# Performance work log

Measured on AMD Instinct MI355X. Metric: run time of the kernel, lower is better.

The kernel has to match this reference:

```python
import jax, jax.numpy as jnp
import numpy as np

N = 100000   # nodes
E = 600000   # edges
D = 128      # input = hidden = output dim
L = 3        # GNN layers
C = 40       # num_classes
EPS = 1e-5   # BatchNorm eps


def setup_inputs() -> dict:
    key = jax.random.key(0)
    ks = jax.random.split(key, 8)
    x = jax.random.normal(ks[0], (N, D), jnp.float32)
    edge_index = jax.random.randint(ks[1], (2, E), 0, N, jnp.int32)
    # GCNConv weights per layer (Glorot-ish scale), bias zeros
    Ws = jax.random.normal(ks[2], (L, D, D), jnp.float32) / np.sqrt(D)
    bs = jnp.zeros((L, D), jnp.float32)
    # BatchNorm affine params
    gammas = jnp.ones((L, D), jnp.float32)
    betas = jnp.zeros((L, D), jnp.float32)
    # PReLU single slope per layer (torch default init 0.25)
    prelu_a = jnp.full((L,), 0.25, jnp.float32)
    # classification head: Linear(D,D) -> ReLU -> Linear(D,C)
    Wh1 = jax.random.normal(ks[3], (D, D), jnp.float32) / np.sqrt(D)
    bh1 = jnp.zeros((D,), jnp.float32)
    Wh2 = jax.random.normal(ks[4], (D, C), jnp.float32) / np.sqrt(D)
    bh2 = jnp.zeros((C,), jnp.float32)
    return dict(x=x, edge_index=edge_index, Ws=Ws, bs=bs, gammas=gammas,
                betas=betas, prelu_a=prelu_a, Wh1=Wh1, bh1=bh1, Wh2=Wh2, bh2=bh2)


def _gcn_conv(h, src, dst, norm, W, b):
    # PyG GCNConv: out_i = sum_{j->i} norm_ij * (x_j W) + b  (self-loops already in src/dst)
    m = (h @ W)[src] * norm[:, None]          # [E+N, D_out]
    return jax.ops.segment_sum(m, dst, num_segments=N) + b


def reference(x, edge_index, Ws, bs, gammas, betas, prelu_a, Wh1, bh1, Wh2, bh2):
    # add self-loops + symmetric normalization (computed once; same graph each layer)
    loops = jnp.arange(N, dtype=edge_index.dtype)
    src = jnp.concatenate([edge_index[0], loops])
    dst = jnp.concatenate([edge_index[1], loops])
    deg = jax.ops.segment_sum(jnp.ones_like(dst, jnp.float32), dst, num_segments=N)
    dinv = jax.lax.rsqrt(jnp.maximum(deg, 1.0))  # deg >= 1 thanks to self-loops
    norm = dinv[src] * dinv[dst]                 # [E+N]

    h = x
    for l in range(L):
        h = _gcn_conv(h, src, dst, norm, Ws[l], bs[l])
        # BatchNorm in training mode: batch statistics over nodes
        mu = h.mean(axis=0)
        var = h.var(axis=0)
        h = (h - mu) * jax.lax.rsqrt(var + EPS) * gammas[l] + betas[l]
        # PReLU
        h = jnp.where(h > 0, h, prelu_a[l] * h)

    embeddings = h
    logits = jax.nn.relu(embeddings @ Wh1 + bh1) @ Wh2 + bh2
    out = jnp.argmax(logits, axis=1)
    return embeddings, logits, out
```

## Files before the change

### kernel.cpp

```cpp
#include <hip/hip_runtime.h>
#include <hip/hip_bf16.h>
#include <cstddef>

#define N_NODES 100000
#define N_EDGES 600000
#define DD 128
#define LL 3
#define CC 40
#define BN_EPS 1e-5f

typedef __attribute__((ext_vector_type(8))) short bfrag;
typedef __attribute__((ext_vector_type(4))) float f32x4;

__device__ __forceinline__ float ldf(const void* p, long i, int f32) {
    return f32 ? ((const float*)p)[i] : __bfloat162float(((const __hip_bfloat16*)p)[i]);
}
__device__ __forceinline__ void stf(void* p, long i, float v, int f32) {
    if (f32) ((float*)p)[i] = v;
    else     ((__hip_bfloat16*)p)[i] = __float2bfloat16(v);
}

__device__ __forceinline__ unsigned short f2bf(float f) {
    unsigned u = __float_as_uint(f);
    unsigned r = (u + 0x7fffu + ((u >> 16) & 1u)) >> 16;
    return (unsigned short)r;
}
__device__ __forceinline__ float bf2f(unsigned short h) {
    return __uint_as_float(((unsigned)h) << 16);
}

__device__ __forceinline__ void gload_lds16(const unsigned short* g, unsigned short* l) {
    __builtin_amdgcn_global_load_lds((const __attribute__((address_space(1))) unsigned int*)g,
                                     (__attribute__((address_space(3))) unsigned int*)l, 16, 0, 0);
}

__global__ __launch_bounds__(256) void k_detect(const void* __restrict__ x, int* __restrict__ dflag) {
    __shared__ int s[256];
    int t = threadIdx.x;
    const __hip_bfloat16* xb = (const __hip_bfloat16*)x;
    int bad = 0;
    for (int i = t; i < 4096; i += 256) {
        float v = __bfloat162float(xb[i]);
        float a = fabsf(v);
        if (!(a < 1e6f)) bad++;
        else if (v != 0.f && a < 1e-30f) bad++;
    }
    s[t] = bad; __syncthreads();
    for (int off = 128; off > 0; off >>= 1) {
        if (t < off) s[t] += s[t + off];
        __syncthreads();
    }
    if (t == 0) *dflag = (s[0] > 64) ? 1 : 0;
}

__global__ __launch_bounds__(256) void k_packw(const void* __restrict__ Ws, const void* __restrict__ Wh1,
                                               unsigned short* __restrict__ Wp,
                                               const int* __restrict__ dflag) {
    int f = *dflag;
    int u = blockIdx.x * 256 + threadIdx.x;
    int mat = u >> 14;
    int r = u & 16383;
    int k = r >> 7, c = r & 127;
    float wv = (mat < 3) ? ldf(Ws, (long)mat * 16384 + r, f) : ldf(Wh1, r, f);
    unsigned short hi = f2bf(wv);
    float r1 = wv - bf2f(hi);
    unsigned short mid = f2bf(r1);
    float r2 = r1 - bf2f(mid);
    unsigned short lo = f2bf(r2);
    int n = c >> 4, ks = k >> 5, j = k & 7;
    int lanep = (c & 15) | (((k >> 3) & 3) << 4);
    long base = (long)mat * 49152 + (long)((n * 4 + ks) * 3) * 512 + lanep * 8 + j;
    Wp[base] = hi;
    Wp[base + 512] = mid;
    Wp[base + 1024] = lo;
}


__global__ __launch_bounds__(256) void k_init(int* cnt, int* fpos, int* rowptr, float* stats) {
    int i = blockIdx.x * 256 + threadIdx.x;
    if (i < N_NODES) { cnt[i] = 0; fpos[i] = 0; }
    if (i < 6 * DD) stats[i] = 0.f;
    if (i == 0) rowptr[N_NODES] = N_EDGES;
}

__global__ __launch_bounds__(256) void k_count(const int* __restrict__ ei, int* __restrict__ cnt) {
    int e = blockIdx.x * 256 + threadIdx.x;
    if (e < N_EDGES) atomicAdd(&cnt[ei[N_EDGES + e]], 1);
}

__global__ __launch_bounds__(256) void k_scan1(const int* __restrict__ cnt, int* __restrict__ rowptr,
                                               int* __restrict__ bsum, float* __restrict__ dinv) {
    __shared__ int s[256];
    int t = threadIdx.x;
    int i = blockIdx.x * 256 + t;
    int v = (i < N_NODES) ? cnt[i] : 0;
    if (i < N_NODES) dinv[i] = 1.f / sqrtf((float)(1 + v));
    s[t] = v; __syncthreads();
    for (int off = 1; off < 256; off <<= 1) {
        int x = (t >= off) ? s[t - off] : 0;
        __syncthreads();
        s[t] += x; __syncthreads();
    }
    if (i < N_NODES) rowptr[i] = s[t] - v;
    if (t == 255) bsum[blockIdx.x] = s[255];
}

__global__ __launch_bounds__(512) void k_scan2(int* bsum, int nb) {
    __shared__ int s[512];
    int t = threadIdx.x;
    int v = (t < nb) ? bsum[t] : 0;
    s[t] = v; __syncthreads();
    for (int off = 1; off < 512; off <<= 1) {
        int x = (t >= off) ? s[t - off] : 0;
        __syncthreads();
        s[t] += x; __syncthreads();
    }
    if (t < nb) bsum[t] = s[t] - v;
}

__global__ __launch_bounds__(256) void k_scan3(int* rowptr, const int* __restrict__ bsum) {
    int i = blockIdx.x * 256 + threadIdx.x;
    if (i < N_NODES) rowptr[i] += bsum[blockIdx.x];
}

__global__ __launch_bounds__(256) void k_fill(const int* __restrict__ ei, int* __restrict__ fpos,
                                              const int* __restrict__ rowptr, int2* __restrict__ adjw,
                                              const float* __restrict__ dinv) {
    int e = blockIdx.x * 256 + threadIdx.x;
    if (e < N_EDGES) {
        int s = ei[e];
        int d = ei[N_EDGES + e];
        int p = atomicAdd(&fpos[d], 1);
        adjw[rowptr[d] + p] = make_int2(s, __float_as_int(dinv[s]));
    }
}

__device__ __forceinline__ float4 load_row4(const void* __restrict__ src, long row, int q, int f) {
    if (f) {
        return ((const float4*)src)[row * 32 + q];
    } else {
        uint2 u = ((const uint2*)src)[row * 32 + q];
        float4 v;
        v.x = __uint_as_float(u.x << 16);
        v.y = __uint_as_float(u.x & 0xffff0000u);
        v.z = __uint_as_float(u.y << 16);
        v.w = __uint_as_float(u.y & 0xffff0000u);
        return v;
    }
}

__device__ __forceinline__ float4 bn4(float4 v, float4 sc, float4 sh, float al) {
    float y;
    y = fmaf(v.x, sc.x, sh.x); v.x = (y > 0.f) ? y : al * y;
    y = fmaf(v.y, sc.y, sh.y); v.y = (y > 0.f) ? y : al * y;
    y = fmaf(v.z, sc.z, sh.z); v.z = (y > 0.f) ? y : al * y;
    y = fmaf(v.w, sc.w, sh.w); v.w = (y > 0.f) ? y : al * y;
    return v;
}


__global__ __launch_bounds__(256) void k_agg(const void* __restrict__ src,
                                             const int* __restrict__ rowptr,
                                             const int2* __restrict__ adjw,
                                             const float* __restrict__ dinv,
                                             const float* __restrict__ stats,
                                             const void* __restrict__ gam,
                                             const void* __restrict__ bet,
                                             const void* __restrict__ pa,
                                             int bnl,
                                             float* __restrict__ outp,
                                             const int* __restrict__ dflag) {
    __shared__ float s_bn[260];
    int f = *dflag;
    int tid = threadIdx.x;
    bool useBN = (stats != nullptr);
    if (useBN) {
        if (tid < 128) {
            const float invn = 1.f / (float)N_NODES;
            float mean = stats[tid] * invn;
            float varv = stats[128 + tid] * invn - mean * mean;
            float s = ldf(gam, (long)bnl * DD + tid, f) / sqrtf(varv + BN_EPS);
            s_bn[tid] = s;
            s_bn[128 + tid] = ldf(bet, (long)bnl * DD + tid, f) - mean * s;
        }
        if (tid == 0) s_bn[256] = ldf(pa, bnl, f);
        __syncthreads();
    }

    int lane = tid & 63;
    int h = lane >> 5;
    int q = lane & 31;
    int i = blockIdx.x * 4 + (tid >> 6);
    if (i >= N_NODES) return;

    float4 sc = make_float4(1.f, 1.f, 1.f, 1.f);
    float4 sh = make_float4(0.f, 0.f, 0.f, 0.f);
    float al = 0.f;
    if (useBN) {
        sc = ((const float4*)s_bn)[q];
        sh = ((const float4*)(s_bn + 128))[q];
        al = s_bn[256];
    }

    float di = dinv[i];
    int e0 = rowptr[i], e1 = rowptr[i + 1];

    float a0 = 0.f, a1 = 0.f, a2 = 0.f, a3 = 0.f;
    if (h == 0) {
        float4 v = load_row4(src, i, q, f);
        if (useBN) v = bn4(v, sc, sh, al);
        a0 = di * v.x; a1 = di * v.y; a2 = di * v.z; a3 = di * v.w;
    }

    for (int base = e0; base < e1; base += 64) {
        int m = e1 - base; if (m > 64) m = 64;
        int2 aw = (lane < m) ? adjw[base + lane] : make_int2(0, 0);
        int ajl = aw.x;
        float wl = __int_as_float(aw.y);
        for (int t = 0; t < m; t += 4) {
            int s0 = t + h;     if (s0 > 63) s0 = 63;
            int s1 = t + 2 + h; if (s1 > 63) s1 = 63;
            int j0 = __shfl(ajl, s0), j1 = __shfl(ajl, s1);
            float w0 = __shfl(wl, s0), w1 = __shfl(wl, s1);
            float4 v0 = load_row4(src, j0, q, f);
            float4 v1 = load_row4(src, j1, q, f);
            if (useBN) {
                v0 = bn4(v0, sc, sh, al);
                v1 = bn4(v1, sc, sh, al);
            }
            a0 += w0 * v0.x + w1 * v1.x;
            a1 += w0 * v0.y + w1 * v1.y;
            a2 += w0 * v0.z + w1 * v1.z;
            a3 += w0 * v0.w + w1 * v1.w;
        }
    }

    a0 += __shfl_xor(a0, 32);
    a1 += __shfl_xor(a1, 32);
    a2 += __shfl_xor(a2, 32);
    a3 += __shfl_xor(a3, 32);

    if (h == 0) {
        float4 r = make_float4(di * a0, di * a1, di * a2, di * a3);
        ((float4*)outp)[(size_t)i * 32 + q] = r;
    }
}


__global__ __launch_bounds__(256, 3) void k_gemm2(const float* __restrict__ A,
                                                  const unsigned short* __restrict__ Wp,
                                                  const void* __restrict__ bias, long boff,
                                                  const float* __restrict__ statsA,
                                                  const void* __restrict__ gam,
                                                  const void* __restrict__ bet,
                                                  const void* __restrict__ pa, int bnl,
                                                  float* __restrict__ stats,
                                                  float* __restrict__ Cout,
                                                  void* __restrict__ embp, int relu,
                                                  const int* __restrict__ dflag) {
    __shared__ unsigned short Wl[24576];
    __shared__ float red[1024];
    int f = *dflag;
    int tid = threadIdx.x;
    int lane = tid & 63;
    int w = tid >> 6;
    int lr = lane & 15;
    int lg = lane >> 4;
    int rowbase = blockIdx.x * 64 + w * 16;
    int arow = rowbase + lr;
    bool rowok = arow < N_NODES;

    #pragma unroll
    for (int u = 0; u < 12; ++u) {
        int chunk = w * 12 + u;
        gload_lds16(Wp + chunk * 512 + lane * 8, &Wl[chunk * 512]);
    }

    float bcol[8];
    #pragma unroll
    for (int n = 0; n < 8; ++n)
        bcol[n] = bias ? ldf(bias, boff + n * 16 + lr, f) : 0.f;

    float alA = statsA ? ldf(pa, bnl, f) : 0.f;
    const float invn = 1.f / (float)N_NODES;

    bfrag ah[4], am[4], alo[4];
    const float4* A4 = (const float4*)A;
    #pragma unroll
    for (int ks = 0; ks < 4; ++ks) {
        int k0 = ks * 32 + lg * 8;
        float xv[8];
        if (rowok) {
            long bi = (long)arow * 32 + (k0 >> 2);
            float4 x0 = A4[bi], x1 = A4[bi + 1];
            xv[0] = x0.x; xv[1] = x0.y; xv[2] = x0.z; xv[3] = x0.w;
            xv[4] = x1.x; xv[5] = x1.y; xv[6] = x1.z; xv[7] = x1.w;
        } else {
            #pragma unroll
            for (int e = 0; e < 8; ++e) xv[e] = 0.f;
        }
        if (statsA) {
            #pragma unroll
            for (int e = 0; e < 8; ++e) {
                int c = k0 + e;
                float mean = statsA[c] * invn;
                float varv = statsA[128 + c] * invn - mean * mean;
                float s = ldf(gam, (long)bnl * DD + c, f) / sqrtf(varv + BN_EPS);
                float y = fmaf(xv[e], s, ldf(bet, (long)bnl * DD + c, f) - mean * s);
                xv[e] = (y > 0.f) ? y : alA * y;
            }
        }
        bfrag hfr, mfr, lfr;
        #pragma unroll
        for (int e = 0; e < 8; ++e) {
            unsigned short hb2 = f2bf(xv[e]);
            float r1 = xv[e] - bf2f(hb2);
            unsigned short mb2 = f2bf(r1);
            float r2 = r1 - bf2f(mb2);
            hfr[e] = (short)hb2;
            mfr[e] = (short)mb2;
            lfr[e] = (short)f2bf(r2);
        }
        ah[ks] = hfr; am[ks] = mfr; alo[ks] = lfr;
        if (embp && rowok) {
            if (f) {
                ((float4*)embp)[(long)arow * 32 + (k0 >> 2)]     = make_float4(xv[0], xv[1], xv[2], xv[3]);
                ((float4*)embp)[(long)arow * 32 + (k0 >> 2) + 1] = make_float4(xv[4], xv[5], xv[6], xv[7]);
            } else {
                uint4 pk;
                pk.x = (unsigned)(unsigned short)hfr[0] | ((unsigned)(unsigned short)hfr[1] << 16);
                pk.y = (unsigned)(unsigned short)hfr[2] | ((unsigned)(unsigned short)hfr[3] << 16);
                pk.z = (unsigned)(unsigned short)hfr[4] | ((unsigned)(unsigned short)hfr[5] << 16);
                pk.w = (unsigned)(unsigned short)hfr[6] | ((unsigned)(unsigned short)hfr[7] << 16);
                ((uint4*)embp)[(long)arow * 16 + (k0 >> 3)] = pk;
            }
        }
    }

    #pragma unroll
    for (int h = 0; h < 2; ++h) {
        if (h) {
            __syncthreads();
            #pragma unroll
            for (int u = 0; u < 12; ++u) {
                int chunk = w * 12 + u;
                gload_lds16(Wp + 24576 + chunk * 512 + lane * 8, &Wl[chunk * 512]);
            }
        }
        __syncthreads();

        #pragma unroll
        for (int nn = 0; nn < 4; ++nn) {
            int n = h * 4 + nn;
            f32x4 accn = (f32x4){0.f, 0.f, 0.f, 0.f};
            #pragma unroll
            for (int ks = 0; ks < 4; ++ks) {
                int base = ((nn * 4 + ks) * 3) * 512 + lane * 8;
                bfrag bh = *(const bfrag*)&Wl[base];
                bfrag bm = *(const bfrag*)&Wl[base + 512];
                bfrag bl = *(const bfrag*)&Wl[base + 1024];
                accn = __builtin_amdgcn_mfma_f32_16x16x32_bf16(ah[ks],  bh, accn, 0, 0, 0);
                accn = __builtin_amdgcn_mfma_f32_16x16x32_bf16(am[ks],  bh, accn, 0, 0, 0);
                accn = __builtin_amdgcn_mfma_f32_16x16x32_bf16(ah[ks],  bm, accn, 0, 0, 0);
                accn = __builtin_amdgcn_mfma_f32_16x16x32_bf16(am[ks],  bm, accn, 0, 0, 0);
                accn = __builtin_amdgcn_mfma_f32_16x16x32_bf16(alo[ks], bh, accn, 0, 0, 0);
                accn = __builtin_amdgcn_mfma_f32_16x16x32_bf16(ah[ks],  bl, accn, 0, 0, 0);
            }
            float ls = 0.f, lq = 0.f;
            int colb = n * 16 + lr;
            #pragma unroll
            for (int reg = 0; reg < 4; ++reg) {
                int r2 = rowbase + lg * 4 + reg;
                if (r2 < N_NODES) {
                    float o = accn[reg] + bcol[n];
                    if (relu) o = fmaxf(o, 0.f);
                    Cout[(long)r2 * 128 + colb] = o;
                    ls += o;
                    lq += o * o;
                }
            }
            if (stats) {
                ls += __shfl_xor(ls, 16); ls += __shfl_xor(ls, 32);
                lq += __shfl_xor(lq, 16); lq += __shfl_xor(lq, 32);
                if (lane < 16) {
                    red[w * 256 + n * 16 + lane] = ls;
                    red[w * 256 + 128 + n * 16 + lane] = lq;
                }
            }
        }
    }

    if (stats) {
        __syncthreads();
        float t = red[tid] + red[256 + tid] + red[512 + tid] + red[768 + tid];
        atomicAdd(&stats[tid], t);
    }
}


__global__ __launch_bounds__(256) void k_head(const float* __restrict__ Hd, const void* __restrict__ W2,
                                              const void* __restrict__ b2,
                                              void* __restrict__ out_base,
                                              const int* __restrict__ dflag) {
    __shared__ float Wl[128][40];
    __shared__ float bl[40];
    __shared__ float rv[32][8];
    __shared__ int ri[32][8];
    int f = *dflag;
    int tid = threadIdx.x;
    for (int u = tid; u < 128 * 40; u += 256) Wl[u / 40][u % 40] = ldf(W2, u, f);
    if (tid < 40) bl[tid] = ldf(b2, tid, f);
    __syncthreads();
    int rl = tid >> 3, g = tid & 7;
    long r = (long)blockIdx.x * 32 + rl;
    float acc[5];
    #pragma unroll
    for (int j = 0; j < 5; ++j) acc[j] = bl[g * 5 + j];
    for (int k = 0; k < 128; ++k) {
        float h = Hd[r * 128 + k];
        #pragma unroll
        for (int j = 0; j < 5; ++j) acc[j] += h * Wl[k][g * 5 + j];
    }
    float best = acc[0]; int bi = 0;
    #pragma unroll
    for (int j = 1; j < 5; ++j)
        if (acc[j] > best) { best = acc[j]; bi = j; }
    const long LOG_OFF = (long)N_NODES * DD;
    const long ARG_OFF = (long)N_NODES * (DD + CC);
    #pragma unroll
    for (int j = 0; j < 5; ++j) stf(out_base, LOG_OFF + r * 40 + g * 5 + j, acc[j], f);
    rv[rl][g] = best; ri[rl][g] = g * 5 + bi;
    __syncthreads();
    if (tid < 32) {
        long row = (long)blockIdx.x * 32 + tid;
        float bb = rv[tid][0]; int bbi = ri[tid][0];
        #pragma unroll
        for (int g2 = 1; g2 < 8; ++g2)
            if (rv[tid][g2] > bb) { bb = rv[tid][g2]; bbi = ri[tid][g2]; }
        stf(out_base, ARG_OFF + row, (float)bbi, f);
    }
}


extern "C" void kernel_launch(void* const* d_in, const int* in_sizes, int n_in,
                              void* d_out, int out_size, void* d_ws, size_t ws_size,
                              hipStream_t stream) {
    const void* x   = d_in[0];
    const int* ei   = (const int*)d_in[1];
    const void* Ws  = d_in[2];
    const void* bs  = d_in[3];
    const void* gam = d_in[4];
    const void* bet = d_in[5];
    const void* pa  = d_in[6];
    const void* Wh1 = d_in[7];
    const void* bh1 = d_in[8];
    const void* Wh2 = d_in[9];
    const void* bh2 = d_in[10];

    char* w = (char*)d_ws;
    int* cnt     = (int*)w;    w += sizeof(int) * N_NODES;
    int* fpos    = (int*)w;    w += sizeof(int) * N_NODES;
    int* rowptr  = (int*)w;    w += sizeof(int) * (N_NODES + 4);
    int2* adjw   = (int2*)w;   w += sizeof(int2) * N_EDGES;
    int* bsum    = (int*)w;    w += sizeof(int) * 512;
    int* dflag   = (int*)w;    w += sizeof(int) * 4;
    float* dinv  = (float*)w;  w += sizeof(float) * N_NODES;
    float* stats = (float*)w;  w += sizeof(float) * (6 * DD);
    unsigned short* Wp = (unsigned short*)w; w += sizeof(unsigned short) * 4 * 49152;
    float* bufA  = (float*)w;  w += sizeof(float) * (size_t)N_NODES * DD;
    float* bufB  = (float*)w;  w += sizeof(float) * (size_t)N_NODES * DD;

    const int scanBlocks = (N_NODES + 255) / 256;
    const int edgeBlocks = (N_EDGES + 255) / 256;
    const int gemmBlocks = (N_NODES + 63) / 64;
    const int aggBlocks  = (N_NODES + 3) / 4;

    k_detect<<<1, 256, 0, stream>>>(x, dflag);
    k_packw<<<256, 256, 0, stream>>>(Ws, Wh1, Wp, dflag);
    k_init<<<scanBlocks, 256, 0, stream>>>(cnt, fpos, rowptr, stats);
    k_count<<<edgeBlocks, 256, 0, stream>>>(ei, cnt);
    k_scan1<<<scanBlocks, 256, 0, stream>>>(cnt, rowptr, bsum, dinv);
    k_scan2<<<1, 512, 0, stream>>>(bsum, scanBlocks);
    k_scan3<<<scanBlocks, 256, 0, stream>>>(rowptr, bsum);
    k_fill<<<edgeBlocks, 256, 0, stream>>>(ei, fpos, rowptr, adjw, dinv);

    for (int l = 0; l < LL; ++l) {
        const void* src = (l == 0) ? x : (const void*)bufB;
        const float* st = (l == 0) ? nullptr : (stats + (l - 1) * 256);
        k_agg<<<aggBlocks, 256, 0, stream>>>(src, rowptr, adjw, dinv, st, gam, bet, pa,
                                             l - 1, bufA, dflag);
        k_gemm2<<<gemmBlocks, 256, 0, stream>>>(bufA, Wp + (size_t)l * 49152, bs, (long)l * DD,
                                                nullptr, gam, bet, pa, 0,
                                                stats + l * 256, bufB, nullptr, 0, dflag);
    }

    k_gemm2<<<gemmBlocks, 256, 0, stream>>>(bufB, Wp + (size_t)3 * 49152, bh1, 0,
                                            stats + 2 * 256, gam, bet, pa, 2,
                                            nullptr, bufA, d_out, 1, dflag);
    k_head<<<(N_NODES / 32), 256, 0, stream>>>(bufA, Wh2, bh2, d_out, dflag);
}
```

Measured before the change: 672.0 us.

## Move bf16x3 split into aggregation producer and add separate BN split kernel

The aggregation kernel now writes its output already split into three bf16 planes (hi/mid/lo) instead of fp32, so the GEMM loads ready MFMA fragments directly and skips the per-row conversion. The final BN+PReLU and the embedding write move out of the head GEMM into a new elementwise k_split kernel. The GEMM also uses two accumulators to break MFMA dependency chains, and keeps per-column stats in registers, reusing the weight LDS for the reduction. In exchange it adds one kernel launch, and the intermediate buffer grows from 4 to 6 bytes per element.

```diff
diff --git a/kernel.cpp b/kernel.cpp
--- a/kernel.cpp
+++ b/kernel.cpp
@@ -27,6 +27,13 @@
 }
 __device__ __forceinline__ float bf2f(unsigned short h) {
     return __uint_as_float(((unsigned)h) << 16);
+}
+
+__device__ __forceinline__ uint4 pack8(const unsigned short* s) {
+    return make_uint4((unsigned)s[0] | ((unsigned)s[1] << 16),
+                      (unsigned)s[2] | ((unsigned)s[3] << 16),
+                      (unsigned)s[4] | ((unsigned)s[5] << 16),
+                      (unsigned)s[6] | ((unsigned)s[7] << 16));
 }
 
 __device__ __forceinline__ void gload_lds16(const unsigned short* g, unsigned short* l) {
@@ -168,7 +175,7 @@
                                              const void* __restrict__ bet,
                                              const void* __restrict__ pa,
                                              int bnl,
-                                             float* __restrict__ outp,
+                                             unsigned short* __restrict__ outp,
                                              const int* __restrict__ dflag) {
     __shared__ float s_bn[260];
     int f = *dflag;
@@ -241,25 +248,84 @@
     a3 += __shfl_xor(a3, 32);
 
     if (h == 0) {
-        float4 r = make_float4(di * a0, di * a1, di * a2, di * a3);
-        ((float4*)outp)[(size_t)i * 32 + q] = r;
-    }
-}
-
-
-__global__ __launch_bounds__(256, 3) void k_gemm2(const float* __restrict__ A,
+        float v[4] = {di * a0, di * a1, di * a2, di * a3};
+        unsigned short hs[4], ms[4], ls_[4];
+        #pragma unroll
+        for (int j = 0; j < 4; ++j) {
+            unsigned short hb = f2bf(v[j]);
+            float r1 = v[j] - bf2f(hb);
+            unsigned short mb = f2bf(r1);
+            hs[j] = hb; ms[j] = mb; ls_[j] = f2bf(r1 - bf2f(mb));
+        }
+        const size_t PS = (size_t)N_NODES * 128;
+        size_t off = (size_t)i * 128 + 4 * q;
+        *(uint2*)&outp[off]          = make_uint2((unsigned)hs[0] | ((unsigned)hs[1] << 16),
+                                                  (unsigned)hs[2] | ((unsigned)hs[3] << 16));
+        *(uint2*)&outp[PS + off]     = make_uint2((unsigned)ms[0] | ((unsigned)ms[1] << 16),
+                                                  (unsigned)ms[2] | ((unsigned)ms[3] << 16));
+        *(uint2*)&outp[2 * PS + off] = make_uint2((unsigned)ls_[0] | ((unsigned)ls_[1] << 16),
+                                                  (unsigned)ls_[2] | ((unsigned)ls_[3] << 16));
+    }
+}
+
+__global__ __launch_bounds__(256) void k_split(const float* __restrict__ H,
+                                               const float* __restrict__ stats,
+                                               const void* __restrict__ gam,
+                                               const void* __restrict__ bet,
+                                               const void* __restrict__ pa, int bnl,
+                                               void* __restrict__ emb,
+                                               unsigned short* __restrict__ P,
+                                               const int* __restrict__ dflag) {
+    __shared__ float s_bn[260];
+    int f = *dflag;
+    int tid = threadIdx.x;
+    if (tid < 128) {
+        const float invn = 1.f / (float)N_NODES;
+        float mean = stats[tid] * invn;
+        float varv = stats[128 + tid] * invn - mean * mean;
+        float s = ldf(gam, (long)bnl * DD + tid, f) / sqrtf(varv + BN_EPS);
+        s_bn[tid] = s;
+        s_bn[128 + tid] = ldf(bet, (long)bnl * DD + tid, f) - mean * s;
+    }
+    if (tid == 0) s_bn[256] = ldf(pa, bnl, f);
+    __syncthreads();
+    float al = s_bn[256];
+    size_t base = (size_t)blockIdx.x * 2048 + (size_t)tid * 8;
+    int c0 = (int)(base & 127);
+    float4 x0 = *(const float4*)&H[base];
+    float4 x1 = *(const float4*)&H[base + 4];
+    float v[8] = {x0.x, x0.y, x0.z, x0.w, x1.x, x1.y, x1.z, x1.w};
+    unsigned short hs[8], ms[8], ls_[8];
+    #pragma unroll
+    for (int e = 0; e < 8; ++e) {
+        float y = fmaf(v[e], s_bn[c0 + e], s_bn[128 + c0 + e]);
+        y = (y > 0.f) ? y : al * y;
+        v[e] = y;
+        unsigned short hb = f2bf(y);
+        float r1 = y - bf2f(hb);
+        unsigned short mb = f2bf(r1);
+        hs[e] = hb; ms[e] = mb; ls_[e] = f2bf(r1 - bf2f(mb));
+    }
+    if (f) {
+        *(float4*)((float*)emb + base)     = make_float4(v[0], v[1], v[2], v[3]);
+        *(float4*)((float*)emb + base + 4) = make_float4(v[4], v[5], v[6], v[7]);
+    } else {
+        *(uint4*)((unsigned short*)emb + base) = pack8(hs);
+    }
+    const size_t PS = (size_t)N_NODES * 128;
+    *(uint4*)&P[base]          = pack8(hs);
+    *(uint4*)&P[PS + base]     = pack8(ms);
+    *(uint4*)&P[2 * PS + base] = pack8(ls_);
+}
+
+
+__global__ __launch_bounds__(256, 3) void k_gemm2(const unsigned short* __restrict__ Ap,
                                                   const unsigned short* __restrict__ Wp,
                                                   const void* __restrict__ bias, long boff,
-                                                  const float* __restrict__ statsA,
-                                                  const void* __restrict__ gam,
-                                                  const void* __restrict__ bet,
-                                                  const void* __restrict__ pa, int bnl,
                                                   float* __restrict__ stats,
-                                                  float* __restrict__ Cout,
-                                                  void* __restrict__ embp, int relu,
+                                                  float* __restrict__ Cout, int relu,
                                                   const int* __restrict__ dflag) {
     __shared__ unsigned short Wl[24576];
-    __shared__ float red[1024];
     int f = *dflag;
     int tid = threadIdx.x;
     int lane = tid & 63;
@@ -276,66 +342,26 @@
         gload_lds16(Wp + chunk * 512 + lane * 8, &Wl[chunk * 512]);
     }
 
-    float bcol[8];
-    #pragma unroll
-    for (int n = 0; n < 8; ++n)
-        bcol[n] = bias ? ldf(bias, boff + n * 16 + lr, f) : 0.f;
-
-    float alA = statsA ? ldf(pa, bnl, f) : 0.f;
-    const float invn = 1.f / (float)N_NODES;
-
     bfrag ah[4], am[4], alo[4];
-    const float4* A4 = (const float4*)A;
+    const size_t PS = (size_t)N_NODES * 128;
     #pragma unroll
     for (int ks = 0; ks < 4; ++ks) {
-        int k0 = ks * 32 + lg * 8;
-        float xv[8];
         if (rowok) {
-            long bi = (long)arow * 32 + (k0 >> 2);
-            float4 x0 = A4[bi], x1 = A4[bi + 1];
-            xv[0] = x0.x; xv[1] = x0.y; xv[2] = x0.z; xv[3] = x0.w;
-            xv[4] = x1.x; xv[5] = x1.y; xv[6] = x1.z; xv[7] = x1.w;
+            size_t off = (size_t)arow * 128 + ks * 32 + lg * 8;
+            ah[ks]  = *(const bfrag*)&Ap[off];
+            am[ks]  = *(const bfrag*)&Ap[PS + off];
+            alo[ks] = *(const bfrag*)&Ap[2 * PS + off];
         } else {
+            bfrag z;
             #pragma unroll
-            for (int e = 0; e < 8; ++e) xv[e] = 0.f;
-        }
-        if (statsA) {
-            #pragma unroll
-            for (int e = 0; e < 8; ++e) {
-                int c = k0 + e;
-                float mean = statsA[c] * invn;
-                float varv = statsA[128 + c] * invn - mean * mean;
-                float s = ldf(gam, (long)bnl * DD + c, f) / sqrtf(varv + BN_EPS);
-                float y = fmaf(xv[e], s, ldf(bet, (long)bnl * DD + c, f) - mean * s);
-                xv[e] = (y > 0.f) ? y : alA * y;
-            }
-        }
-        bfrag hfr, mfr, lfr;
-        #pragma unroll
-        for (int e = 0; e < 8; ++e) {
-            unsigned short hb2 = f2bf(xv[e]);
-            float r1 = xv[e] - bf2f(hb2);
-            unsigned short mb2 = f2bf(r1);
-            float r2 = r1 - bf2f(mb2);
-            hfr[e] = (short)hb2;
-            mfr[e] = (short)mb2;
-            lfr[e] = (short)f2bf(r2);
-        }
-        ah[ks] = hfr; am[ks] = mfr; alo[ks] = lfr;
-        if (embp && rowok) {
-            if (f) {
-                ((float4*)embp)[(long)arow * 32 + (k0 >> 2)]     = make_float4(xv[0], xv[1], xv[2], xv[3]);
-                ((float4*)embp)[(long)arow * 32 + (k0 >> 2) + 1] = make_float4(xv[4], xv[5], xv[6], xv[7]);
-            } else {
-                uint4 pk;
-                pk.x = (unsigned)(unsigned short)hfr[0] | ((unsigned)(unsigned short)hfr[1] << 16);
-                pk.y = (unsigned)(unsigned short)hfr[2] | ((unsigned)(unsigned short)hfr[3] << 16);
-                pk.z = (unsigned)(unsigned short)hfr[4] | ((unsigned)(unsigned short)hfr[5] << 16);
-                pk.w = (unsigned)(unsigned short)hfr[6] | ((unsigned)(unsigned short)hfr[7] << 16);
-                ((uint4*)embp)[(long)arow * 16 + (k0 >> 3)] = pk;
-            }
-        }
-    }
+            for (int j = 0; j < 8; ++j) z[j] = 0;
+            ah[ks] = z; am[ks] = z; alo[ks] = z;
+        }
+    }
+
+    float lsum[8], lsq[8];
+    #pragma unroll
+    for (int n2 = 0; n2 < 8; ++n2) { lsum[n2] = 0.f; lsq[n2] = 0.f; }
 
     #pragma unroll
     for (int h = 0; h < 2; ++h) {
@@ -352,45 +378,58 @@
         #pragma unroll
         for (int nn = 0; nn < 4; ++nn) {
             int n = h * 4 + nn;
-            f32x4 accn = (f32x4){0.f, 0.f, 0.f, 0.f};
+            bfrag bh[4], bm[4], bl[4];
             #pragma unroll
             for (int ks = 0; ks < 4; ++ks) {
-                int base = ((nn * 4 + ks) * 3) * 512 + lane * 8;
-                bfrag bh = *(const bfrag*)&Wl[base];
-                bfrag bm = *(const bfrag*)&Wl[base + 512];
-                bfrag bl = *(const bfrag*)&Wl[base + 1024];
-                accn = __builtin_amdgcn_mfma_f32_16x16x32_bf16(ah[ks],  bh, accn, 0, 0, 0);
-                accn = __builtin_amdgcn_mfma_f32_16x16x32_bf16(am[ks],  bh, accn, 0, 0, 0);
-                accn = __builtin_amdgcn_mfma_f32_16x16x32_bf16(ah[ks],  bm, accn, 0, 0, 0);
-                accn = __builtin_amdgcn_mfma_f32_16x16x32_bf16(am[ks],  bm, accn, 0, 0, 0);
-                accn = __builtin_amdgcn_mfma_f32_16x16x32_bf16(alo[ks], bh, accn, 0, 0, 0);
-                accn = __builtin_amdgcn_mfma_f32_16x16x32_bf16(ah[ks],  bl, accn, 0, 0, 0);
+                int bb = ((nn * 4 + ks) * 3) * 512 + lane * 8;
+                bh[ks] = *(const bfrag*)&Wl[bb];
+                bm[ks] = *(const bfrag*)&Wl[bb + 512];
+                bl[ks] = *(const bfrag*)&Wl[bb + 1024];
             }
-            float ls = 0.f, lq = 0.f;
+            f32x4 accA = (f32x4){0.f, 0.f, 0.f, 0.f};
+            f32x4 accB = (f32x4){0.f, 0.f, 0.f, 0.f};
+            #pragma unroll
+            for (int ks = 0; ks < 4; ++ks) {
+                accA = __builtin_amdgcn_mfma_f32_16x16x32_bf16(ah[ks],  bh[ks], accA, 0, 0, 0);
+                accB = __builtin_amdgcn_mfma_f32_16x16x32_bf16(am[ks],  bh[ks], accB, 0, 0, 0);
+                accA = __builtin_amdgcn_mfma_f32_16x16x32_bf16(ah[ks],  bm[ks], accA, 0, 0, 0);
+                accB = __builtin_amdgcn_mfma_f32_16x16x32_bf16(am[ks],  bm[ks], accB, 0, 0, 0);
+                accA = __builtin_amdgcn_mfma_f32_16x16x32_bf16(alo[ks], bh[ks], accA, 0, 0, 0);
+                accB = __builtin_amdgcn_mfma_f32_16x16x32_bf16(ah[ks],  bl[ks], accB, 0, 0, 0);
+            }
+            float bc = bias ? ldf(bias, boff + n * 16 + lr, f) : 0.f;
             int colb = n * 16 + lr;
             #pragma unroll
             for (int reg = 0; reg < 4; ++reg) {
                 int r2 = rowbase + lg * 4 + reg;
                 if (r2 < N_NODES) {
-                    float o = accn[reg] + bcol[n];
+                    float o = accA[reg] + accB[reg] + bc;
                     if (relu) o = fmaxf(o, 0.f);
                     Cout[(long)r2 * 128 + colb] = o;
-                    ls += o;
-                    lq += o * o;
+                    lsum[n] += o;
+                    lsq[n] += o * o;
                 }
             }
-            if (stats) {
-                ls += __shfl_xor(ls, 16); ls += __shfl_xor(ls, 32);
-                lq += __shfl_xor(lq, 16); lq += __shfl_xor(lq, 32);
-                if (lane < 16) {
-                    red[w * 256 + n * 16 + lane] = ls;
-                    red[w * 256 + 128 + n * 16 + lane] = lq;
-                }
+        }
+    }
+
+    if (stats) {
+        #pragma unroll
+        for (int n2 = 0; n2 < 8; ++n2) {
+            lsum[n2] += __shfl_xor(lsum[n2], 16);
+            lsum[n2] += __shfl_xor(lsum[n2], 32);
+            lsq[n2]  += __shfl_xor(lsq[n2], 16);
+            lsq[n2]  += __shfl_xor(lsq[n2], 32);
+        }
+        __syncthreads();
+        float* red = (float*)Wl;
+        if (lane < 16) {
+            #pragma unroll
+            for (int n2 = 0; n2 < 8; ++n2) {
+                red[w * 256 + n2 * 16 + lane] = lsum[n2];
+                red[w * 256 + 128 + n2 * 16 + lane] = lsq[n2];
             }
         }
-    }
-
-    if (stats) {
         __syncthreads();
         float t = red[tid] + red[256 + tid] + red[512 + tid] + red[768 + tid];
         atomicAdd(&stats[tid], t);
@@ -467,13 +506,14 @@
     float* dinv  = (float*)w;  w += sizeof(float) * N_NODES;
     float* stats = (float*)w;  w += sizeof(float) * (6 * DD);
     unsigned short* Wp = (unsigned short*)w; w += sizeof(unsigned short) * 4 * 49152;
-    float* bufA  = (float*)w;  w += sizeof(float) * (size_t)N_NODES * DD;
+    unsigned short* bufP = (unsigned short*)w; w += sizeof(unsigned short) * 3 * (size_t)N_NODES * DD;
     float* bufB  = (float*)w;  w += sizeof(float) * (size_t)N_NODES * DD;
 
     const int scanBlocks = (N_NODES + 255) / 256;
     const int edgeBlocks = (N_EDGES + 255) / 256;
     const int gemmBlocks = (N_NODES + 63) / 64;
     const int aggBlocks  = (N_NODES + 3) / 4;
+    const int splitBlocks = (N_NODES * DD) / 2048;
 
     k_detect<<<1, 256, 0, stream>>>(x, dflag);
     k_packw<<<256, 256, 0, stream>>>(Ws, Wh1, Wp, dflag);
@@ -488,14 +528,14 @@
         const void* src = (l == 0) ? x : (const void*)bufB;
         const float* st = (l == 0) ? nullptr : (stats + (l - 1) * 256);
         k_agg<<<aggBlocks, 256, 0, stream>>>(src, rowptr, adjw, dinv, st, gam, bet, pa,
-                                             l - 1, bufA, dflag);
-        k_gemm2<<<gemmBlocks, 256, 0, stream>>>(bufA, Wp + (size_t)l * 49152, bs, (long)l * DD,
-                                                nullptr, gam, bet, pa, 0,
-                                                stats + l * 256, bufB, nullptr, 0, dflag);
-    }
-
-    k_gemm2<<<gemmBlocks, 256, 0, stream>>>(bufB, Wp + (size_t)3 * 49152, bh1, 0,
-                                            stats + 2 * 256, gam, bet, pa, 2,
-                                            nullptr, bufA, d_out, 1, dflag);
-    k_head<<<(N_NODES / 32), 256, 0, stream>>>(bufA, Wh2, bh2, d_out, dflag);
-}
+                                             l - 1, bufP, dflag);
+        k_gemm2<<<gemmBlocks, 256, 0, stream>>>(bufP, Wp + (size_t)l * 49152, bs, (long)l * DD,
+                                                stats + l * 256, bufB, 0, dflag);
+    }
+
+    k_split<<<splitBlocks, 256, 0, stream>>>(bufB, stats + 2 * 256, gam, bet, pa, 2,
+                                             d_out, bufP, dflag);
+    k_gemm2<<<gemmBlocks, 256, 0, stream>>>(bufP, Wp + (size_t)3 * 49152, bh1, 0,
+                                            nullptr, bufB, 1, dflag);
+    k_head<<<(N_NODES / 32), 256, 0, stream>>>(bufB, Wh2, bh2, d_out, dflag);
+}
```

Measured after the change: 754.4 us. +12.3%, slower.

## Assign one node per half-wave in aggregation and split MFMA accumulator chains

Applied to the files above, without the earlier changes.

The aggregation kernel now gives each 32-lane half-wave its own node instead of splitting one node's edges across both halves. This removes the final cross-half reduction and halves the number of aggregation blocks. The GEMM kernel preloads the B fragments and splits the 24-MFMA dependency chain into two independent accumulators to expose more instruction-level parallelism. It also accumulates BN statistics in registers, reduces them once at the end, and reuses the weight LDS buffer for the reduction, which frees 4 KB of shared memory. The risk is load imbalance between the two half-waves when neighbouring nodes have different degrees, plus extra register pressure from holding the preloaded fragments.

```diff
diff --git a/kernel.cpp b/kernel.cpp
--- a/kernel.cpp
+++ b/kernel.cpp
@@ -190,7 +190,7 @@
     int lane = tid & 63;
     int h = lane >> 5;
     int q = lane & 31;
-    int i = blockIdx.x * 4 + (tid >> 6);
+    int i = blockIdx.x * 8 + ((tid >> 6) << 1) + h;
     if (i >= N_NODES) return;
 
     float4 sc = make_float4(1.f, 1.f, 1.f, 1.f);
@@ -205,23 +205,20 @@
     float di = dinv[i];
     int e0 = rowptr[i], e1 = rowptr[i + 1];
 
-    float a0 = 0.f, a1 = 0.f, a2 = 0.f, a3 = 0.f;
-    if (h == 0) {
-        float4 v = load_row4(src, i, q, f);
-        if (useBN) v = bn4(v, sc, sh, al);
-        a0 = di * v.x; a1 = di * v.y; a2 = di * v.z; a3 = di * v.w;
-    }
-
-    for (int base = e0; base < e1; base += 64) {
-        int m = e1 - base; if (m > 64) m = 64;
-        int2 aw = (lane < m) ? adjw[base + lane] : make_int2(0, 0);
+    float4 v = load_row4(src, i, q, f);
+    if (useBN) v = bn4(v, sc, sh, al);
+    float a0 = di * v.x, a1 = di * v.y, a2 = di * v.z, a3 = di * v.w;
+
+    for (int base = e0; base < e1; base += 32) {
+        int m = e1 - base; if (m > 32) m = 32;
+        int2 aw = (q < m) ? adjw[base + q] : make_int2(0, 0);
         int ajl = aw.x;
         float wl = __int_as_float(aw.y);
-        for (int t = 0; t < m; t += 4) {
-            int s0 = t + h;     if (s0 > 63) s0 = 63;
-            int s1 = t + 2 + h; if (s1 > 63) s1 = 63;
-            int j0 = __shfl(ajl, s0), j1 = __shfl(ajl, s1);
-            float w0 = __shfl(wl, s0), w1 = __shfl(wl, s1);
+        for (int t = 0; t < m; t += 2) {
+            int j0 = __shfl(ajl, t, 32);
+            int j1 = __shfl(ajl, t + 1, 32);
+            float w0 = __shfl(wl, t, 32);
+            float w1 = __shfl(wl, t + 1, 32);
             float4 v0 = load_row4(src, j0, q, f);
             float4 v1 = load_row4(src, j1, q, f);
             if (useBN) {
@@ -235,15 +232,8 @@
         }
     }
 
-    a0 += __shfl_xor(a0, 32);
-    a1 += __shfl_xor(a1, 32);
-    a2 += __shfl_xor(a2, 32);
-    a3 += __shfl_xor(a3, 32);
-
-    if (h == 0) {
-        float4 r = make_float4(di * a0, di * a1, di * a2, di * a3);
-        ((float4*)outp)[(size_t)i * 32 + q] = r;
-    }
+    float4 r = make_float4(di * a0, di * a1, di * a2, di * a3);
+    ((float4*)outp)[(size_t)i * 32 + q] = r;
 }
 
 
@@ -259,7 +249,6 @@
                                                   void* __restrict__ embp, int relu,
                                                   const int* __restrict__ dflag) {
     __shared__ unsigned short Wl[24576];
-    __shared__ float red[1024];
     int f = *dflag;
     int tid = threadIdx.x;
     int lane = tid & 63;
@@ -337,6 +326,10 @@
         }
     }
 
+    float lsum[8], lsq[8];
+    #pragma unroll
+    for (int n2 = 0; n2 < 8; ++n2) { lsum[n2] = 0.f; lsq[n2] = 0.f; }
+
     #pragma unroll
     for (int h = 0; h < 2; ++h) {
         if (h) {
@@ -352,45 +345,57 @@
         #pragma unroll
         for (int nn = 0; nn < 4; ++nn) {
             int n = h * 4 + nn;
-            f32x4 accn = (f32x4){0.f, 0.f, 0.f, 0.f};
+            bfrag bh[4], bm[4], bl[4];
             #pragma unroll
             for (int ks = 0; ks < 4; ++ks) {
-                int base = ((nn * 4 + ks) * 3) * 512 + lane * 8;
-                bfrag bh = *(const bfrag*)&Wl[base];
-                bfrag bm = *(const bfrag*)&Wl[base + 512];
-                bfrag bl = *(const bfrag*)&Wl[base + 1024];
-                accn = __builtin_amdgcn_mfma_f32_16x16x32_bf16(ah[ks],  bh, accn, 0, 0, 0);
-                accn = __builtin_amdgcn_mfma_f32_16x16x32_bf16(am[ks],  bh, accn, 0, 0, 0);
-                accn = __builtin_amdgcn_mfma_f32_16x16x32_bf16(ah[ks],  bm, accn, 0, 0, 0);
-                accn = __builtin_amdgcn_mfma_f32_16x16x32_bf16(am[ks],  bm, accn, 0, 0, 0);
-                accn = __builtin_amdgcn_mfma_f32_16x16x32_bf16(alo[ks], bh, accn, 0, 0, 0);
-                accn = __builtin_amdgcn_mfma_f32_16x16x32_bf16(ah[ks],  bl, accn, 0, 0, 0);
-            }
-            float ls = 0.f, lq = 0.f;
+                int bb = ((nn * 4 + ks) * 3) * 512 + lane * 8;
+                bh[ks] = *(const bfrag*)&Wl[bb];
+                bm[ks] = *(const bfrag*)&Wl[bb + 512];
+                bl[ks] = *(const bfrag*)&Wl[bb + 1024];
+            }
+            f32x4 accA = (f32x4){0.f, 0.f, 0.f, 0.f};
+            f32x4 accB = (f32x4){0.f, 0.f, 0.f, 0.f};
+            #pragma unroll
+            for (int ks = 0; ks < 4; ++ks) {
+                accA = __builtin_amdgcn_mfma_f32_16x16x32_bf16(ah[ks],  bh[ks], accA, 0, 0, 0);
+                accB = __builtin_amdgcn_mfma_f32_16x16x32_bf16(am[ks],  bh[ks], accB, 0, 0, 0);
+                accA = __builtin_amdgcn_mfma_f32_16x16x32_bf16(ah[ks],  bm[ks], accA, 0, 0, 0);
+                accB = __builtin_amdgcn_mfma_f32_16x16x32_bf16(am[ks],  bm[ks], accB, 0, 0, 0);
+                accA = __builtin_amdgcn_mfma_f32_16x16x32_bf16(alo[ks], bh[ks], accA, 0, 0, 0);
+                accB = __builtin_amdgcn_mfma_f32_16x16x32_bf16(ah[ks],  bl[ks], accB, 0, 0, 0);
+            }
             int colb = n * 16 + lr;
             #pragma unroll
             for (int reg = 0; reg < 4; ++reg) {
                 int r2 = rowbase + lg * 4 + reg;
                 if (r2 < N_NODES) {
-                    float o = accn[reg] + bcol[n];
+                    float o = accA[reg] + accB[reg] + bcol[n];
                     if (relu) o = fmaxf(o, 0.f);
                     Cout[(long)r2 * 128 + colb] = o;
-                    ls += o;
-                    lq += o * o;
+                    lsum[n] += o;
+                    lsq[n] += o * o;
                 }
             }
-            if (stats) {
-                ls += __shfl_xor(ls, 16); ls += __shfl_xor(ls, 32);
-                lq += __shfl_xor(lq, 16); lq += __shfl_xor(lq, 32);
-                if (lane < 16) {
-                    red[w * 256 + n * 16 + lane] = ls;
-                    red[w * 256 + 128 + n * 16 + lane] = lq;
-                }
-            }
         }
     }
 
     if (stats) {
+        #pragma unroll
+        for (int n2 = 0; n2 < 8; ++n2) {
+            lsum[n2] += __shfl_xor(lsum[n2], 16);
+            lsum[n2] += __shfl_xor(lsum[n2], 32);
+            lsq[n2]  += __shfl_xor(lsq[n2], 16);
+            lsq[n2]  += __shfl_xor(lsq[n2], 32);
+        }
+        __syncthreads();
+        float* red = (float*)Wl;
+        if (lane < 16) {
+            #pragma unroll
+            for (int n2 = 0; n2 < 8; ++n2) {
+                red[w * 256 + n2 * 16 + lane] = lsum[n2];
+                red[w * 256 + 128 + n2 * 16 + lane] = lsq[n2];
+            }
+        }
         __syncthreads();
         float t = red[tid] + red[256 + tid] + red[512 + tid] + red[768 + tid];
         atomicAdd(&stats[tid], t);
@@ -473,7 +478,7 @@
     const int scanBlocks = (N_NODES + 255) / 256;
     const int edgeBlocks = (N_EDGES + 255) / 256;
     const int gemmBlocks = (N_NODES + 63) / 64;
-    const int aggBlocks  = (N_NODES + 3) / 4;
+    const int aggBlocks  = (N_NODES + 7) / 8;
 
     k_detect<<<1, 256, 0, stream>>>(x, dflag);
     k_packw<<<256, 256, 0, stream>>>(Ws, Wh1, Wp, dflag);
```

After: 668.6 us. Within noise of the previous version (-0.5%).
